# Kernel optimization log

Measured on AMD Instinct MI355X. Metric: run time of the kernel, lower is better.

## Reference

```python
import jax, jax.numpy as jnp
import numpy as np

D_MODEL = 256
D_STATE = 16
D_CONV = 4
EXPAND = 2
D_INNER = EXPAND * D_MODEL  # 512
DT_RANK = (D_MODEL + 15) // 16  # 16
D_FF = 4 * D_MODEL  # 1024
BATCH, SEQ = 16, 2048
EPS = 1e-12


def layer_norm(x, g, b):
    mu = jnp.mean(x, axis=-1, keepdims=True)
    var = jnp.mean(jnp.square(x - mu), axis=-1, keepdims=True)
    return (x - mu) * jax.lax.rsqrt(var + EPS) * g + b


def setup_inputs() -> dict:
    key = jax.random.key(0)
    ks = jax.random.split(key, 16)
    s = lambda n: 1.0 / np.sqrt(n)
    inp = {
        "x": jax.random.normal(ks[0], (BATCH, SEQ, D_MODEL), dtype=jnp.float32),
        "in_proj_w": jax.random.normal(ks[1], (2 * D_INNER, D_MODEL)) * s(D_MODEL),
        "conv_w": jax.random.normal(ks[2], (D_INNER, 1, D_CONV)) * s(D_CONV),
        "conv_b": jax.random.normal(ks[3], (D_INNER,)) * 0.02,
        "x_proj_w": jax.random.normal(ks[4], (DT_RANK + 2 * D_STATE, D_INNER)) * s(D_INNER),
        "dt_proj_w": jax.random.normal(ks[5], (D_INNER, DT_RANK)) * s(DT_RANK),
        "dt_proj_b": jnp.log(jnp.expm1(0.01 * jnp.ones((D_INNER,)))),  # softplus^-1(0.01)
        "A_log": jnp.log(jnp.broadcast_to(jnp.arange(1, D_STATE + 1, dtype=jnp.float32), (D_INNER, D_STATE))),
        "Dskip": jnp.ones((D_INNER,)),
        "out_proj_w": jax.random.normal(ks[6], (D_MODEL, D_INNER)) * s(D_INNER),
        "ln1_g": jnp.ones((D_MODEL,)), "ln1_b": jnp.zeros((D_MODEL,)),
        "w1": jax.random.normal(ks[7], (D_FF, D_MODEL)) * s(D_MODEL),
        "b1": jnp.zeros((D_FF,)),
        "w2": jax.random.normal(ks[8], (D_MODEL, D_FF)) * s(D_FF),
        "b2": jnp.zeros((D_MODEL,)),
        "ln2_g": jnp.ones((D_MODEL,)), "ln2_b": jnp.zeros((D_MODEL,)),
    }
    return inp


def _mamba(x, in_proj_w, conv_w, conv_b, x_proj_w, dt_proj_w, dt_proj_b, A_log, Dskip, out_proj_w):
    B, L, _ = x.shape
    xz = jnp.einsum('bld,ed->ble', x, in_proj_w)  # [B,L,2*D_INNER]
    u, z = jnp.split(xz, 2, axis=-1)
    # depthwise causal conv1d over sequence
    uc = jax.lax.conv_general_dilated(
        u.transpose(0, 2, 1), conv_w, window_strides=(1,),
        padding=[(D_CONV - 1, 0)], feature_group_count=D_INNER,
        dimension_numbers=('NCH', 'OIH', 'NCH'))
    uc = jax.nn.silu(uc + conv_b[None, :, None]).transpose(0, 2, 1)  # [B,L,D_INNER]
    x_dbl = jnp.einsum('blc,ec->ble', uc, x_proj_w)
    dt, Bmat, Cmat = jnp.split(x_dbl, [DT_RANK, DT_RANK + D_STATE], axis=-1)
    delta = jax.nn.softplus(jnp.einsum('blr,cr->blc', dt, dt_proj_w) + dt_proj_b)  # [B,L,D_INNER]
    A = -jnp.exp(A_log)  # [D_INNER, D_STATE]

    def step(h, inp):
        d_t, B_t, C_t, u_t = inp  # [B,dI],[B,N],[B,N],[B,dI]
        dA = jnp.exp(d_t[..., None] * A)                      # [B,dI,N]
        h = h * dA + (d_t * u_t)[..., None] * B_t[:, None, :]  # [B,dI,N]
        y = jnp.sum(h * C_t[:, None, :], axis=-1)              # [B,dI]
        return h, y

    h0 = jnp.zeros((B, D_INNER, D_STATE), dtype=x.dtype)
    xs = (delta.transpose(1, 0, 2), Bmat.transpose(1, 0, 2), Cmat.transpose(1, 0, 2), uc.transpose(1, 0, 2))
    _, ys = jax.lax.scan(step, h0, xs)
    y = ys.transpose(1, 0, 2) + uc * Dskip  # [B,L,D_INNER]
    y = y * jax.nn.silu(z)
    return jnp.einsum('blc,dc->bld', y, out_proj_w)


def reference(x, in_proj_w, conv_w, conv_b, x_proj_w, dt_proj_w, dt_proj_b, A_log, Dskip,
              out_proj_w, ln1_g, ln1_b, w1, b1, w2, b2, ln2_g, ln2_b):
    # MambaLayer.forward, eval mode (dropout = identity), num_layers > 1 -> residual
    h = _mamba(x, in_proj_w, conv_w, conv_b, x_proj_w, dt_proj_w, dt_proj_b, A_log, Dskip, out_proj_w)
    h = layer_norm(h + x, ln1_g, ln1_b)
    # FeedForward: GELU MLP with residual + LayerNorm
    ff = jax.nn.gelu(jnp.einsum('bld,fd->blf', h, w1) + b1, approximate=False)
    ff = jnp.einsum('blf,df->bld', ff, w2) + b2
    return layer_norm(ff + h, ln2_g, ln2_b)
```

## Files before the change

### kernel.cpp

```cpp
#include <hip/hip_runtime.h>
#include <cmath>

#define S_TOTAL 32768
#define LSEQ    2048
#define NBATCH  16
#define DM      256
#define DI      512
#define DSTATE  16
#define DTRANK  16
#define NCHUNK  16
#define CHUNK   128

typedef __attribute__((ext_vector_type(8))) short short8;
typedef __attribute__((ext_vector_type(4))) float f32x4;

__device__ __forceinline__ unsigned short f2bf(float f) {
    union { float f; unsigned int u; } v; v.f = f;
    const unsigned int r = v.u + 0x7fffu + ((v.u >> 16) & 1u);
    return (unsigned short)(r >> 16);
}
__device__ __forceinline__ float bf2f(unsigned short h) {
    union { unsigned int u; float f; } v; v.u = ((unsigned int)h) << 16;
    return v.f;
}
__device__ __forceinline__ float gelu_exact(float x) {
    return 0.5f * x * (1.0f + erff(x * 0.70710678118654752440f));
}
__device__ __forceinline__ float softplus_fast(float x) {
    return fmaxf(x, 0.0f) + __logf(1.0f + __expf(-fabsf(x)));
}

enum { EPI_NONE = 0, EPI_GELU_BIAS = 1, EPI_RESID16 = 2, EPI_BIAS_RESID16 = 3 };

template <int EPI, bool OUTBF>
__global__ __launch_bounds__(256, 4) void gemm_bf16(
    const unsigned short* __restrict__ A, int lda,
    const unsigned short* __restrict__ W, int ldw,
    const float* __restrict__ bias,
    const unsigned short* __restrict__ resid, int ldr,
    void* __restrict__ Cout, int ldc, int nstore,
    int K, int nclampW)
{
    __shared__ unsigned short lds[2][2][4096];

    const int tid = threadIdx.x;
    const int w = tid >> 6, l = tid & 63;
    const int brow = blockIdx.y * 128, bcol = blockIdx.x * 128;
    const int wr = w >> 1, wc = w & 1;
    const int lr = l & 15, lh = l >> 4;

    f32x4 acc[4][4];
    #pragma unroll
    for (int m = 0; m < 4; ++m)
        #pragma unroll
        for (int n = 0; n < 4; ++n)
            acc[m][n] = f32x4{0.f, 0.f, 0.f, 0.f};

    auto stage = [&](int buf, int k0) {
        const int gslot = (l & 3) ^ ((l >> 2) & 3) ^ ((l >> 4) & 3);
        #pragma unroll
        for (int i = 0; i < 2; ++i) {
            const int row = i * 64 + w * 16 + (l >> 2);
            {
                const unsigned short* g =
                    A + (size_t)(brow + row) * lda + k0 + gslot * 8;
                const unsigned short* lp = &lds[buf][0][i * 2048 + w * 512];
                __builtin_amdgcn_global_load_lds(
                    (const __attribute__((address_space(1))) void*)g,
                    (__attribute__((address_space(3))) void*)lp, 16, 0, 0);
            }
            {
                int grow = bcol + row; if (grow > nclampW) grow = nclampW;
                const unsigned short* g =
                    W + (size_t)grow * ldw + k0 + gslot * 8;
                const unsigned short* lp = &lds[buf][1][i * 2048 + w * 512];
                __builtin_amdgcn_global_load_lds(
                    (const __attribute__((address_space(1))) void*)g,
                    (__attribute__((address_space(3))) void*)lp, 16, 0, 0);
            }
        }
    };

    stage(0, 0);

    const int nkt = K >> 5;
    for (int t = 0; t < nkt; ++t) {
        if (t + 1 < nkt) {
            stage((t + 1) & 1, (t + 1) << 5);
            __builtin_amdgcn_sched_barrier(0);
            asm volatile("s_waitcnt vmcnt(4)" ::: "memory");
        } else {
            __builtin_amdgcn_sched_barrier(0);
            asm volatile("s_waitcnt vmcnt(0)" ::: "memory");
        }
        __builtin_amdgcn_s_barrier();
        __builtin_amdgcn_sched_barrier(0);

        const unsigned short* la = &lds[t & 1][0][0];
        const unsigned short* lb = &lds[t & 1][1][0];
        short8 af[4], bw[4];
        #pragma unroll
        for (int m = 0; m < 4; ++m) {
            const int row = wr * 64 + m * 16 + lr;
            const int slot = lh ^ (row & 3) ^ ((row >> 2) & 3);
            af[m] = *(const short8*)(la + row * 32 + slot * 8);
        }
        #pragma unroll
        for (int n = 0; n < 4; ++n) {
            const int row = wc * 64 + n * 16 + lr;
            const int slot = lh ^ (row & 3) ^ ((row >> 2) & 3);
            bw[n] = *(const short8*)(lb + row * 32 + slot * 8);
        }
        #pragma unroll
        for (int m = 0; m < 4; ++m)
            #pragma unroll
            for (int n = 0; n < 4; ++n)
                acc[m][n] = __builtin_amdgcn_mfma_f32_16x16x32_bf16(
                    af[m], bw[n], acc[m][n], 0, 0, 0);

        __builtin_amdgcn_sched_barrier(0);
        asm volatile("s_waitcnt lgkmcnt(0)" ::: "memory");
        __builtin_amdgcn_s_barrier();
        __builtin_amdgcn_sched_barrier(0);
    }

    #pragma unroll
    for (int m = 0; m < 4; ++m) {
        #pragma unroll
        for (int j = 0; j < 4; ++j) {
            const int rg = brow + wr * 64 + m * 16 + lh * 4 + j;
            #pragma unroll
            for (int n = 0; n < 4; ++n) {
                const int cg = bcol + wc * 64 + n * 16 + lr;
                if (cg < nstore) {
                    float v = acc[m][n][j];
                    if (EPI == EPI_GELU_BIAS) {
                        v = gelu_exact(v + bias[cg]);
                    } else if (EPI == EPI_RESID16) {
                        v += bf2f(resid[(size_t)rg * ldr + cg]);
                    } else if (EPI == EPI_BIAS_RESID16) {
                        v += bias[cg] + bf2f(resid[(size_t)rg * ldr + cg]);
                    }
                    if (OUTBF)
                        ((unsigned short*)Cout)[(size_t)rg * ldc + cg] = f2bf(v);
                    else
                        ((float*)Cout)[(size_t)rg * ldc + cg] = v;
                }
            }
        }
    }
}

__global__ __launch_bounds__(256) void convert_kernel(
    const float* __restrict__ x,   const float* __restrict__ win,
    const float* __restrict__ wxp, const float* __restrict__ wop,
    const float* __restrict__ w1,  const float* __restrict__ w2,
    unsigned short* __restrict__ x16, unsigned short* __restrict__ wb)
{
    int idx = blockIdx.x * 256 + threadIdx.x;
    const int NX = S_TOTAL * DM;
    if (idx < NX) { x16[idx] = f2bf(x[idx]); return; }
    idx -= NX;
    if (idx < 262144) { wb[idx] = f2bf(win[idx]); return; }
    idx -= 262144;
    if (idx < 24576)  { wb[262144 + idx] = f2bf(wxp[idx]); return; }
    idx -= 24576;
    if (idx < 131072) { wb[286720 + idx] = f2bf(wop[idx]); return; }
    idx -= 131072;
    if (idx < 262144) { wb[417792 + idx] = f2bf(w1[idx]); return; }
    idx -= 262144;
    if (idx < 262144) { wb[679936 + idx] = f2bf(w2[idx]); return; }
}

__global__ __launch_bounds__(256) void conv_silu_kernel(
    const unsigned short* __restrict__ uz, const float* __restrict__ cw,
    const float* __restrict__ cb, unsigned short* __restrict__ uch)
{
    const int idx = blockIdx.x * 256 + threadIdx.x;
    const int g = idx & 63;
    const int s = idx >> 6;
    const int l = s & (LSEQ - 1);
    const int c0 = g * 8;

    float acc[8];
    float4 cwv[8];
    #pragma unroll
    for (int j = 0; j < 8; ++j) {
        acc[j] = cb[c0 + j];
        cwv[j] = *(const float4*)(cw + (c0 + j) * 4);
    }
    #pragma unroll
    for (int t = 0; t < 4; ++t) {
        const int lt = l - 3 + t;
        if (lt >= 0) {
            const short8 uv = *(const short8*)(uz + (s - 3 + t) * 1024 + c0);
            #pragma unroll
            for (int j = 0; j < 8; ++j) {
                const float wt = (t == 0) ? cwv[j].x : (t == 1) ? cwv[j].y
                               : (t == 2) ? cwv[j].z : cwv[j].w;
                acc[j] += bf2f((unsigned short)uv[j]) * wt;
            }
        }
    }
    short8 ob;
    #pragma unroll
    for (int j = 0; j < 8; ++j) {
        const float sig = 1.0f / (1.0f + __expf(-acc[j]));
        ob[j] = (short)f2bf(acc[j] * sig);
    }
    *(short8*)(uch + s * DI + c0) = ob;
}

__global__ __launch_bounds__(256) void scan_p1(
    const unsigned short* __restrict__ uch, const float* __restrict__ xdbl,
    const float* __restrict__ dtw, const float* __restrict__ dtb,
    const float* __restrict__ A_log,
    float* __restrict__ P, float* __restrict__ Q)
{
    const int tid = threadIdx.x;
    const int cg = blockIdx.x & 7, k = (blockIdx.x >> 3) & 15, b = blockIdx.x >> 7;
    const int c = (cg << 6) + (tid >> 2), nq = (tid & 3) << 2;

    const float4 al = *(const float4*)(A_log + c * DSTATE + nq);
    const float4 a4 = {-__expf(al.x), -__expf(al.y), -__expf(al.z), -__expf(al.w)};
    const float4 dw4 = *(const float4*)(dtw + c * DTRANK + nq);
    const float dtbc = dtb[c];

    float4 h4 = {0, 0, 0, 0};
    float sumd = 0.f;

    const int base = (b * LSEQ + k * CHUNK) * DI + c;
    const int xb   = (b * LSEQ + k * CHUNK) * 64 + nq;

    float  uA_ = bf2f(uch[base]);
    float4 TA_ = *(const float4*)(xdbl + xb);
    float4 BA_ = *(const float4*)(xdbl + xb + DTRANK);
    float  uB_ = bf2f(uch[base + DI]);
    float4 TB_ = *(const float4*)(xdbl + xb + 64);
    float4 BB_ = *(const float4*)(xdbl + xb + 64 + DTRANK);

    for (int l = 0; l < CHUNK; l += 2) {
        const int lc = (l + 2 < CHUNK) ? (l + 2) : (CHUNK - 2);
        const int o2 = base + lc * DI;
        const int x2 = xb + lc * 64;
        const float  uC_ = bf2f(uch[o2]);
        const float  uD_ = bf2f(uch[o2 + DI]);
        const float4 TC_ = *(const float4*)(xdbl + x2);
        const float4 BC_ = *(const float4*)(xdbl + x2 + DTRANK);
        const float4 TD_ = *(const float4*)(xdbl + x2 + 64);
        const float4 BD_ = *(const float4*)(xdbl + x2 + 64 + DTRANK);

        {
            float pd = TA_.x * dw4.x + TA_.y * dw4.y + TA_.z * dw4.z + TA_.w * dw4.w;
            pd += __shfl_xor(pd, 1);
            pd += __shfl_xor(pd, 2);
            const float d = softplus_fast(pd + dtbc);
            const float4 e = {__expf(d * a4.x), __expf(d * a4.y),
                              __expf(d * a4.z), __expf(d * a4.w)};
            const float du = d * uA_;
            h4.x = h4.x * e.x + du * BA_.x;
            h4.y = h4.y * e.y + du * BA_.y;
            h4.z = h4.z * e.z + du * BA_.z;
            h4.w = h4.w * e.w + du * BA_.w;
            sumd += d;
        }
        {
            float pd = TB_.x * dw4.x + TB_.y * dw4.y + TB_.z * dw4.z + TB_.w * dw4.w;
            pd += __shfl_xor(pd, 1);
            pd += __shfl_xor(pd, 2);
            const float d = softplus_fast(pd + dtbc);
            const float4 e = {__expf(d * a4.x), __expf(d * a4.y),
                              __expf(d * a4.z), __expf(d * a4.w)};
            const float du = d * uB_;
            h4.x = h4.x * e.x + du * BB_.x;
            h4.y = h4.y * e.y + du * BB_.y;
            h4.z = h4.z * e.z + du * BB_.z;
            h4.w = h4.w * e.w + du * BB_.w;
            sumd += d;
        }
        uA_ = uC_; TA_ = TC_; BA_ = BC_;
        uB_ = uD_; TB_ = TD_; BB_ = BD_;
    }

    const int pi = ((b * NCHUNK + k) * DI + c) * 16 + nq;
    const float4 P4 = {__expf(a4.x * sumd), __expf(a4.y * sumd),
                       __expf(a4.z * sumd), __expf(a4.w * sumd)};
    *(float4*)(P + pi) = P4;
    *(float4*)(Q + pi) = h4;
}

__global__ __launch_bounds__(256) void scan_p2(
    const float* __restrict__ P, const float* __restrict__ Q,
    float* __restrict__ HS)
{
    const int t  = blockIdx.x * 256 + threadIdx.x;
    const int nq = (t & 3) << 2;
    const int c  = (t >> 2) & (DI - 1);
    const int b  = t >> 11;
    float4 hs = {0, 0, 0, 0};
    for (int k = 0; k < NCHUNK; ++k) {
        const int idx = ((b * NCHUNK + k) * DI + c) * 16 + nq;
        if (k > 0) {
            const int ip = idx - DI * 16;
            const float4 p4 = *(const float4*)(P + ip);
            const float4 q4 = *(const float4*)(Q + ip);
            hs.x = hs.x * p4.x + q4.x;
            hs.y = hs.y * p4.y + q4.y;
            hs.z = hs.z * p4.z + q4.z;
            hs.w = hs.w * p4.w + q4.w;
        }
        *(float4*)(HS + idx) = hs;
    }
}

__global__ __launch_bounds__(256) void scan_p3(
    const unsigned short* __restrict__ uch, const float* __restrict__ xdbl,
    const float* __restrict__ dtw, const float* __restrict__ dtb,
    const unsigned short* __restrict__ zuz,
    const float* __restrict__ A_log, const float* __restrict__ Dskip,
    const float* __restrict__ HS, unsigned short* __restrict__ y)
{
    const int tid = threadIdx.x;
    const int cg = blockIdx.x & 7, k = (blockIdx.x >> 3) & 15, b = blockIdx.x >> 7;
    const int c = (cg << 6) + (tid >> 2), nq = (tid & 3) << 2;

    const float4 al = *(const float4*)(A_log + c * DSTATE + nq);
    const float4 a4 = {-__expf(al.x), -__expf(al.y), -__expf(al.z), -__expf(al.w)};
    const float4 dw4 = *(const float4*)(dtw + c * DTRANK + nq);
    const float dtbc = dtb[c];
    const float dsk = Dskip[c];

    const int pi = ((b * NCHUNK + k) * DI + c) * 16 + nq;
    float4 h4 = *(const float4*)(HS + pi);

    const int base = (b * LSEQ + k * CHUNK) * DI + c;
    const int xb   = (b * LSEQ + k * CHUNK) * 64 + nq;
    const int zb   = (b * LSEQ + k * CHUNK) * 1024 + c;

    float  uA_ = bf2f(uch[base]);
    float  zA_ = bf2f(zuz[zb]);
    float4 TA_ = *(const float4*)(xdbl + xb);
    float4 BA_ = *(const float4*)(xdbl + xb + DTRANK);
    float4 CA_ = *(const float4*)(xdbl + xb + 32);
    float  uB_ = bf2f(uch[base + DI]);
    float  zB_ = bf2f(zuz[zb + 1024]);
    float4 TB_ = *(const float4*)(xdbl + xb + 64);
    float4 BB_ = *(const float4*)(xdbl + xb + 64 + DTRANK);
    float4 CB_ = *(const float4*)(xdbl + xb + 64 + 32);

    for (int l = 0; l < CHUNK; l += 2) {
        const int lc = (l + 2 < CHUNK) ? (l + 2) : (CHUNK - 2);
        const int o2 = base + lc * DI;
        const int x2 = xb + lc * 64;
        const int z2 = zb + lc * 1024;
        const float  uC_ = bf2f(uch[o2]);
        const float  uD_ = bf2f(uch[o2 + DI]);
        const float  zC_ = bf2f(zuz[z2]);
        const float  zD_ = bf2f(zuz[z2 + 1024]);
        const float4 TC_ = *(const float4*)(xdbl + x2);
        const float4 BC_ = *(const float4*)(xdbl + x2 + DTRANK);
        const float4 CC_ = *(const float4*)(xdbl + x2 + 32);
        const float4 TD_ = *(const float4*)(xdbl + x2 + 64);
        const float4 BD_ = *(const float4*)(xdbl + x2 + 64 + DTRANK);
        const float4 CD_ = *(const float4*)(xdbl + x2 + 64 + 32);

        {
            float pd = TA_.x * dw4.x + TA_.y * dw4.y + TA_.z * dw4.z + TA_.w * dw4.w;
            pd += __shfl_xor(pd, 1);
            pd += __shfl_xor(pd, 2);
            const float d = softplus_fast(pd + dtbc);
            const float4 e = {__expf(d * a4.x), __expf(d * a4.y),
                              __expf(d * a4.z), __expf(d * a4.w)};
            const float du = d * uA_;
            h4.x = h4.x * e.x + du * BA_.x;
            h4.y = h4.y * e.y + du * BA_.y;
            h4.z = h4.z * e.z + du * BA_.z;
            h4.w = h4.w * e.w + du * BA_.w;
            float yp = h4.x * CA_.x + h4.y * CA_.y + h4.z * CA_.z + h4.w * CA_.w;
            yp += __shfl_xor(yp, 1);
            yp += __shfl_xor(yp, 2);
            if ((tid & 3) == 0) {
                const float sg = 1.0f / (1.0f + __expf(-zA_));
                y[base + l * DI] = f2bf((yp + uA_ * dsk) * (zA_ * sg));
            }
        }
        {
            float pd = TB_.x * dw4.x + TB_.y * dw4.y + TB_.z * dw4.z + TB_.w * dw4.w;
            pd += __shfl_xor(pd, 1);
            pd += __shfl_xor(pd, 2);
            const float d = softplus_fast(pd + dtbc);
            const float4 e = {__expf(d * a4.x), __expf(d * a4.y),
                              __expf(d * a4.z), __expf(d * a4.w)};
            const float du = d * uB_;
            h4.x = h4.x * e.x + du * BB_.x;
            h4.y = h4.y * e.y + du * BB_.y;
            h4.z = h4.z * e.z + du * BB_.z;
            h4.w = h4.w * e.w + du * BB_.w;
            float yp = h4.x * CB_.x + h4.y * CB_.y + h4.z * CB_.z + h4.w * CB_.w;
            yp += __shfl_xor(yp, 1);
            yp += __shfl_xor(yp, 2);
            if ((tid & 3) == 0) {
                const float sg = 1.0f / (1.0f + __expf(-zB_));
                y[base + (l + 1) * DI] = f2bf((yp + uB_ * dsk) * (zB_ * sg));
            }
        }
        uA_ = uC_; zA_ = zC_; TA_ = TC_; BA_ = BC_; CA_ = CC_;
        uB_ = uD_; zB_ = zD_; TB_ = TD_; BB_ = BD_; CB_ = CD_;
    }
}

__global__ __launch_bounds__(256) void layernorm256_kernel(
    const float* __restrict__ in, const float* __restrict__ g,
    const float* __restrict__ b, float* __restrict__ out,
    unsigned short* __restrict__ out16)
{
    const int wave = threadIdx.x >> 6;
    const int lane = threadIdx.x & 63;
    const int row  = blockIdx.x * 4 + wave;

    const float4 v = ((const float4*)(in + (size_t)row * DM))[lane];
    float s  = v.x + v.y + v.z + v.w;
    float sq = v.x * v.x + v.y * v.y + v.z * v.z + v.w * v.w;
    #pragma unroll
    for (int o = 1; o < 64; o <<= 1) {
        s  += __shfl_xor(s, o);
        sq += __shfl_xor(sq, o);
    }
    const float mu  = s * (1.0f / 256.0f);
    const float var = sq * (1.0f / 256.0f) - mu * mu;
    const float rs  = rsqrtf(var + 1e-12f);

    const float4 gg = ((const float4*)g)[lane];
    const float4 bb = ((const float4*)b)[lane];
    float4 o4;
    o4.x = (v.x - mu) * rs * gg.x + bb.x;
    o4.y = (v.y - mu) * rs * gg.y + bb.y;
    o4.z = (v.z - mu) * rs * gg.z + bb.z;
    o4.w = (v.w - mu) * rs * gg.w + bb.w;
    if (out)
        ((float4*)(out + (size_t)row * DM))[lane] = o4;
    if (out16) {
        uint2 p;
        p.x = (unsigned int)f2bf(o4.x) | ((unsigned int)f2bf(o4.y) << 16);
        p.y = (unsigned int)f2bf(o4.z) | ((unsigned int)f2bf(o4.w) << 16);
        *(uint2*)(out16 + (size_t)row * DM + lane * 4) = p;
    }
}

extern "C" void kernel_launch(void* const* d_in, const int* in_sizes, int n_in,
                              void* d_out, int out_size, void* d_ws, size_t ws_size,
                              hipStream_t stream)
{
    const float* x          = (const float*)d_in[0];
    const float* in_proj_w  = (const float*)d_in[1];
    const float* conv_w     = (const float*)d_in[2];
    const float* conv_b     = (const float*)d_in[3];
    const float* x_proj_w   = (const float*)d_in[4];
    const float* dt_proj_w  = (const float*)d_in[5];
    const float* dt_proj_b  = (const float*)d_in[6];
    const float* A_log      = (const float*)d_in[7];
    const float* Dskip      = (const float*)d_in[8];
    const float* out_proj_w = (const float*)d_in[9];
    const float* ln1_g      = (const float*)d_in[10];
    const float* ln1_b      = (const float*)d_in[11];
    const float* w1         = (const float*)d_in[12];
    const float* b1         = (const float*)d_in[13];
    const float* w2         = (const float*)d_in[14];
    const float* b2         = (const float*)d_in[15];
    const float* ln2_g      = (const float*)d_in[16];
    const float* ln2_b      = (const float*)d_in[17];
    float* out = (float*)d_out;
    char*  ws8 = (char*)d_ws;

    const size_t Mi = 1048576;
    unsigned short* bufUZ  = (unsigned short*)(ws8);
    unsigned short* bufUCh = (unsigned short*)(ws8 + 64 * Mi);
    float*          bufXD  = (float*)(ws8 + 96 * Mi);
    unsigned short* bufFF  = (unsigned short*)(ws8 + 104 * Mi);
    float*          bufP   = (float*)(ws8 + 168 * Mi);
    float*          bufQ   = (float*)(ws8 + 176 * Mi);
    float*          bufHS  = (float*)(ws8 + 184 * Mi);
    unsigned short* wb     = (unsigned short*)(ws8 + 192 * Mi);

    float*          bufM   = (float*)(ws8);
    float*          bufF2  = (float*)(ws8 + 32 * Mi);
    unsigned short* bufH1h = (unsigned short*)(ws8 + 168 * Mi);
    unsigned short* bufY   = bufUCh;

    unsigned short* wInP16 = wb;
    unsigned short* wXP16  = wb + 262144;
    unsigned short* wOP16  = wb + 286720;
    unsigned short* wW116  = wb + 417792;
    unsigned short* wW216  = wb + 679936;

    unsigned short* x16 = (unsigned short*)d_out;

    const dim3 blk(256);
    const int MT = S_TOTAL / 128;

    convert_kernel<<<dim3(36448), blk, 0, stream>>>(
        x, in_proj_w, x_proj_w, out_proj_w, w1, w2, x16, wb);

    gemm_bf16<EPI_NONE, true><<<dim3(8, MT), blk, 0, stream>>>(
        x16, DM, wInP16, DM, nullptr, nullptr, 0, bufUZ, 1024, 1024, DM, 1023);

    conv_silu_kernel<<<dim3(S_TOTAL * 64 / 256), blk, 0, stream>>>(
        bufUZ, conv_w, conv_b, bufUCh);

    gemm_bf16<EPI_NONE, false><<<dim3(1, MT), blk, 0, stream>>>(
        bufUCh, DI, wXP16, DI, nullptr, nullptr, 0, bufXD, 64, 64, DI, 47);

    scan_p1<<<dim3(NBATCH * NCHUNK * 8), blk, 0, stream>>>(
        bufUCh, bufXD, dt_proj_w, dt_proj_b, A_log, bufP, bufQ);
    scan_p2<<<dim3(NBATCH * DI * 4 / 256), blk, 0, stream>>>(
        bufP, bufQ, bufHS);
    scan_p3<<<dim3(NBATCH * NCHUNK * 8), blk, 0, stream>>>(
        bufUCh, bufXD, dt_proj_w, dt_proj_b, bufUZ + 512, A_log, Dskip,
        bufHS, bufY);

    gemm_bf16<EPI_RESID16, false><<<dim3(2, MT), blk, 0, stream>>>(
        bufY, DI, wOP16, DI, nullptr, x16, DM, bufM, DM, 256, DI, 255);

    layernorm256_kernel<<<dim3(S_TOTAL / 4), blk, 0, stream>>>(
        bufM, ln1_g, ln1_b, nullptr, bufH1h);

    gemm_bf16<EPI_GELU_BIAS, true><<<dim3(8, MT), blk, 0, stream>>>(
        bufH1h, DM, wW116, DM, b1, nullptr, 0, bufFF, 1024, 1024, DM, 1023);

    gemm_bf16<EPI_BIAS_RESID16, false><<<dim3(2, MT), blk, 0, stream>>>(
        bufFF, 1024, wW216, 1024, b2, bufH1h, DM, bufF2, DM, 256, 1024, 255);

    layernorm256_kernel<<<dim3(S_TOTAL / 4), blk, 0, stream>>>(
        bufF2, ln2_g, ln2_b, out, nullptr);
}
```

Measured before the change: 647.7 us.

## Precompute delta via a softplus GEMM and restructure scan for more chunks

Delta is now computed once by a new bf16 GEMM (dt_proj with fused softplus-bias epilogue) on the low-rank part of x_proj output, which the x_proj GEMM also writes as bf16 through a new aux output. The scan kernels read precomputed bf16 delta instead of recomputing the dt dot product, softplus and shuffles in both passes. The scan now uses 64-step chunks (32 chunks) with 2 lanes per channel, each holding 8 states, which reduces per-step shuffles and doubles the chunk parallelism. In exchange it adds an extra kernel and bf16 rounding of delta, and it writes and reads a 32MB delta buffer.

```diff
diff --git a/kernel.cpp b/kernel.cpp
--- a/kernel.cpp
+++ b/kernel.cpp
@@ -8,8 +8,8 @@
 #define DI      512
 #define DSTATE  16
 #define DTRANK  16
-#define NCHUNK  16
-#define CHUNK   128
+#define NCHUNK  32
+#define CHUNK   64
 
 typedef __attribute__((ext_vector_type(8))) short short8;
 typedef __attribute__((ext_vector_type(4))) float f32x4;
@@ -30,7 +30,8 @@
     return fmaxf(x, 0.0f) + __logf(1.0f + __expf(-fabsf(x)));
 }
 
-enum { EPI_NONE = 0, EPI_GELU_BIAS = 1, EPI_RESID16 = 2, EPI_BIAS_RESID16 = 3 };
+enum { EPI_NONE = 0, EPI_GELU_BIAS = 1, EPI_RESID16 = 2, EPI_BIAS_RESID16 = 3,
+       EPI_SOFTPLUS_BIAS = 4 };
 
 template <int EPI, bool OUTBF>
 __global__ __launch_bounds__(256, 4) void gemm_bf16(
@@ -39,7 +40,8 @@
     const float* __restrict__ bias,
     const unsigned short* __restrict__ resid, int ldr,
     void* __restrict__ Cout, int ldc, int nstore,
-    int K, int nclampW)
+    int K, int nclampW,
+    unsigned short* __restrict__ aux, int auxn)
 {
     __shared__ unsigned short lds[2][2][4096];
 
@@ -140,11 +142,15 @@
                         v += bf2f(resid[(size_t)rg * ldr + cg]);
                     } else if (EPI == EPI_BIAS_RESID16) {
                         v += bias[cg] + bf2f(resid[(size_t)rg * ldr + cg]);
+                    } else if (EPI == EPI_SOFTPLUS_BIAS) {
+                        v = softplus_fast(v + bias[cg]);
                     }
                     if (OUTBF)
                         ((unsigned short*)Cout)[(size_t)rg * ldc + cg] = f2bf(v);
                     else
                         ((float*)Cout)[(size_t)rg * ldc + cg] = v;
+                    if (aux && cg < auxn)
+                        aux[(size_t)rg * auxn + cg] = f2bf(v);
                 }
             }
         }
@@ -155,6 +161,7 @@
     const float* __restrict__ x,   const float* __restrict__ win,
     const float* __restrict__ wxp, const float* __restrict__ wop,
     const float* __restrict__ w1,  const float* __restrict__ w2,
+    const float* __restrict__ dtw,
     unsigned short* __restrict__ x16, unsigned short* __restrict__ wb)
 {
     int idx = blockIdx.x * 256 + threadIdx.x;
@@ -170,6 +177,12 @@
     if (idx < 262144) { wb[417792 + idx] = f2bf(w1[idx]); return; }
     idx -= 262144;
     if (idx < 262144) { wb[679936 + idx] = f2bf(w2[idx]); return; }
+    idx -= 262144;
+    if (idx < 16384) {
+        const int r = idx >> 5, q = idx & 31;
+        wb[942080 + idx] = (q < DTRANK) ? f2bf(dtw[r * DTRANK + q])
+                                        : (unsigned short)0;
+    }
 }
 
 __global__ __launch_bounds__(256) void conv_silu_kernel(
@@ -212,81 +225,75 @@
 }
 
 __global__ __launch_bounds__(256) void scan_p1(
-    const unsigned short* __restrict__ uch, const float* __restrict__ xdbl,
-    const float* __restrict__ dtw, const float* __restrict__ dtb,
-    const float* __restrict__ A_log,
+    const unsigned short* __restrict__ uch,
+    const unsigned short* __restrict__ delh,
+    const float* __restrict__ xdbl, const float* __restrict__ A_log,
     float* __restrict__ P, float* __restrict__ Q)
 {
     const int tid = threadIdx.x;
-    const int cg = blockIdx.x & 7, k = (blockIdx.x >> 3) & 15, b = blockIdx.x >> 7;
-    const int c = (cg << 6) + (tid >> 2), nq = (tid & 3) << 2;
-
-    const float4 al = *(const float4*)(A_log + c * DSTATE + nq);
-    const float4 a4 = {-__expf(al.x), -__expf(al.y), -__expf(al.z), -__expf(al.w)};
-    const float4 dw4 = *(const float4*)(dtw + c * DTRANK + nq);
-    const float dtbc = dtb[c];
-
-    float4 h4 = {0, 0, 0, 0};
+    const int w = tid >> 6, lane = tid & 63;
+    const int cgb = blockIdx.x & 3;
+    const int k = (blockIdx.x >> 2) & (NCHUNK - 1);
+    const int b = blockIdx.x >> 7;
+    const int c = cgb * 128 + w * 32 + (lane >> 1);
+    const int nb = (lane & 1) * 8;
+
+    float a4[8];
+    {
+        const float4 a0 = *(const float4*)(A_log + c * DSTATE + nb);
+        const float4 a1 = *(const float4*)(A_log + c * DSTATE + nb + 4);
+        a4[0] = -__expf(a0.x); a4[1] = -__expf(a0.y);
+        a4[2] = -__expf(a0.z); a4[3] = -__expf(a0.w);
+        a4[4] = -__expf(a1.x); a4[5] = -__expf(a1.y);
+        a4[6] = -__expf(a1.z); a4[7] = -__expf(a1.w);
+    }
+    float h[8] = {};
     float sumd = 0.f;
 
-    const int base = (b * LSEQ + k * CHUNK) * DI + c;
-    const int xb   = (b * LSEQ + k * CHUNK) * 64 + nq;
-
-    float  uA_ = bf2f(uch[base]);
-    float4 TA_ = *(const float4*)(xdbl + xb);
-    float4 BA_ = *(const float4*)(xdbl + xb + DTRANK);
-    float  uB_ = bf2f(uch[base + DI]);
-    float4 TB_ = *(const float4*)(xdbl + xb + 64);
-    float4 BB_ = *(const float4*)(xdbl + xb + 64 + DTRANK);
+    const int s0 = b * LSEQ + k * CHUNK;
+    const unsigned short* pu = uch + s0 * DI + c;
+    const unsigned short* pd = delh + s0 * DI + c;
+    const float* px = xdbl + s0 * 64 + DTRANK + nb;
+
+    unsigned short dA = pd[0], uA = pu[0];
+    float BA[8];
+    *(float4*)&BA[0] = *(const float4*)(px);
+    *(float4*)&BA[4] = *(const float4*)(px + 4);
 
     for (int l = 0; l < CHUNK; l += 2) {
-        const int lc = (l + 2 < CHUNK) ? (l + 2) : (CHUNK - 2);
-        const int o2 = base + lc * DI;
-        const int x2 = xb + lc * 64;
-        const float  uC_ = bf2f(uch[o2]);
-        const float  uD_ = bf2f(uch[o2 + DI]);
-        const float4 TC_ = *(const float4*)(xdbl + x2);
-        const float4 BC_ = *(const float4*)(xdbl + x2 + DTRANK);
-        const float4 TD_ = *(const float4*)(xdbl + x2 + 64);
-        const float4 BD_ = *(const float4*)(xdbl + x2 + 64 + DTRANK);
-
+        const unsigned short dB = pd[DI], uB = pu[DI];
+        float BB[8];
+        *(float4*)&BB[0] = *(const float4*)(px + 64);
+        *(float4*)&BB[4] = *(const float4*)(px + 68);
         {
-            float pd = TA_.x * dw4.x + TA_.y * dw4.y + TA_.z * dw4.z + TA_.w * dw4.w;
-            pd += __shfl_xor(pd, 1);
-            pd += __shfl_xor(pd, 2);
-            const float d = softplus_fast(pd + dtbc);
-            const float4 e = {__expf(d * a4.x), __expf(d * a4.y),
-                              __expf(d * a4.z), __expf(d * a4.w)};
-            const float du = d * uA_;
-            h4.x = h4.x * e.x + du * BA_.x;
-            h4.y = h4.y * e.y + du * BA_.y;
-            h4.z = h4.z * e.z + du * BA_.z;
-            h4.w = h4.w * e.w + du * BA_.w;
+            const float d = bf2f(dA), u = bf2f(uA);
+            const float du = d * u;
+            #pragma unroll
+            for (int i = 0; i < 8; ++i)
+                h[i] = h[i] * __expf(d * a4[i]) + du * BA[i];
             sumd += d;
         }
+        pu += 2 * DI; pd += 2 * DI; px += 128;
+        dA = pd[0]; uA = pu[0];
+        *(float4*)&BA[0] = *(const float4*)(px);
+        *(float4*)&BA[4] = *(const float4*)(px + 4);
         {
-            float pd = TB_.x * dw4.x + TB_.y * dw4.y + TB_.z * dw4.z + TB_.w * dw4.w;
-            pd += __shfl_xor(pd, 1);
-            pd += __shfl_xor(pd, 2);
-            const float d = softplus_fast(pd + dtbc);
-            const float4 e = {__expf(d * a4.x), __expf(d * a4.y),
-                              __expf(d * a4.z), __expf(d * a4.w)};
-            const float du = d * uB_;
-            h4.x = h4.x * e.x + du * BB_.x;
-            h4.y = h4.y * e.y + du * BB_.y;
-            h4.z = h4.z * e.z + du * BB_.z;
-            h4.w = h4.w * e.w + du * BB_.w;
+            const float d = bf2f(dB), u = bf2f(uB);
+            const float du = d * u;
+            #pragma unroll
+            for (int i = 0; i < 8; ++i)
+                h[i] = h[i] * __expf(d * a4[i]) + du * BB[i];
             sumd += d;
         }
-        uA_ = uC_; TA_ = TC_; BA_ = BC_;
-        uB_ = uD_; TB_ = TD_; BB_ = BD_;
-    }
-
-    const int pi = ((b * NCHUNK + k) * DI + c) * 16 + nq;
-    const float4 P4 = {__expf(a4.x * sumd), __expf(a4.y * sumd),
-                       __expf(a4.z * sumd), __expf(a4.w * sumd)};
-    *(float4*)(P + pi) = P4;
-    *(float4*)(Q + pi) = h4;
+    }
+
+    const int pi = ((b * NCHUNK + k) * DI + c) * 16 + nb;
+    *(float4*)(P + pi) = make_float4(__expf(a4[0] * sumd), __expf(a4[1] * sumd),
+                                     __expf(a4[2] * sumd), __expf(a4[3] * sumd));
+    *(float4*)(P + pi + 4) = make_float4(__expf(a4[4] * sumd), __expf(a4[5] * sumd),
+                                         __expf(a4[6] * sumd), __expf(a4[7] * sumd));
+    *(float4*)(Q + pi) = make_float4(h[0], h[1], h[2], h[3]);
+    *(float4*)(Q + pi + 4) = make_float4(h[4], h[5], h[6], h[7]);
 }
 
 __global__ __launch_bounds__(256) void scan_p2(
@@ -314,98 +321,94 @@
 }
 
 __global__ __launch_bounds__(256) void scan_p3(
-    const unsigned short* __restrict__ uch, const float* __restrict__ xdbl,
-    const float* __restrict__ dtw, const float* __restrict__ dtb,
-    const unsigned short* __restrict__ zuz,
+    const unsigned short* __restrict__ uch,
+    const unsigned short* __restrict__ delh,
+    const float* __restrict__ xdbl, const unsigned short* __restrict__ zuz,
     const float* __restrict__ A_log, const float* __restrict__ Dskip,
     const float* __restrict__ HS, unsigned short* __restrict__ y)
 {
     const int tid = threadIdx.x;
-    const int cg = blockIdx.x & 7, k = (blockIdx.x >> 3) & 15, b = blockIdx.x >> 7;
-    const int c = (cg << 6) + (tid >> 2), nq = (tid & 3) << 2;
-
-    const float4 al = *(const float4*)(A_log + c * DSTATE + nq);
-    const float4 a4 = {-__expf(al.x), -__expf(al.y), -__expf(al.z), -__expf(al.w)};
-    const float4 dw4 = *(const float4*)(dtw + c * DTRANK + nq);
-    const float dtbc = dtb[c];
+    const int w = tid >> 6, lane = tid & 63;
+    const int cgb = blockIdx.x & 3;
+    const int k = (blockIdx.x >> 2) & (NCHUNK - 1);
+    const int b = blockIdx.x >> 7;
+    const int c = cgb * 128 + w * 32 + (lane >> 1);
+    const int nb = (lane & 1) * 8;
+
+    float a4[8];
+    {
+        const float4 a0 = *(const float4*)(A_log + c * DSTATE + nb);
+        const float4 a1 = *(const float4*)(A_log + c * DSTATE + nb + 4);
+        a4[0] = -__expf(a0.x); a4[1] = -__expf(a0.y);
+        a4[2] = -__expf(a0.z); a4[3] = -__expf(a0.w);
+        a4[4] = -__expf(a1.x); a4[5] = -__expf(a1.y);
+        a4[6] = -__expf(a1.z); a4[7] = -__expf(a1.w);
+    }
     const float dsk = Dskip[c];
 
-    const int pi = ((b * NCHUNK + k) * DI + c) * 16 + nq;
-    float4 h4 = *(const float4*)(HS + pi);
-
-    const int base = (b * LSEQ + k * CHUNK) * DI + c;
-    const int xb   = (b * LSEQ + k * CHUNK) * 64 + nq;
-    const int zb   = (b * LSEQ + k * CHUNK) * 1024 + c;
-
-    float  uA_ = bf2f(uch[base]);
-    float  zA_ = bf2f(zuz[zb]);
-    float4 TA_ = *(const float4*)(xdbl + xb);
-    float4 BA_ = *(const float4*)(xdbl + xb + DTRANK);
-    float4 CA_ = *(const float4*)(xdbl + xb + 32);
-    float  uB_ = bf2f(uch[base + DI]);
-    float  zB_ = bf2f(zuz[zb + 1024]);
-    float4 TB_ = *(const float4*)(xdbl + xb + 64);
-    float4 BB_ = *(const float4*)(xdbl + xb + 64 + DTRANK);
-    float4 CB_ = *(const float4*)(xdbl + xb + 64 + 32);
+    const int pi = ((b * NCHUNK + k) * DI + c) * 16 + nb;
+    float h[8];
+    *(float4*)&h[0] = *(const float4*)(HS + pi);
+    *(float4*)&h[4] = *(const float4*)(HS + pi + 4);
+
+    const int s0 = b * LSEQ + k * CHUNK;
+    const unsigned short* pu = uch + s0 * DI + c;
+    const unsigned short* pd = delh + s0 * DI + c;
+    const unsigned short* pz = zuz + s0 * 1024 + c;
+    const float* px = xdbl + s0 * 64 + DTRANK + nb;
+    unsigned short* py = y + s0 * DI + c;
+
+    unsigned short dA = pd[0], uA = pu[0], zA = pz[0];
+    float BA[8], CA[8];
+    *(float4*)&BA[0] = *(const float4*)(px);
+    *(float4*)&BA[4] = *(const float4*)(px + 4);
+    *(float4*)&CA[0] = *(const float4*)(px + DSTATE);
+    *(float4*)&CA[4] = *(const float4*)(px + DSTATE + 4);
 
     for (int l = 0; l < CHUNK; l += 2) {
-        const int lc = (l + 2 < CHUNK) ? (l + 2) : (CHUNK - 2);
-        const int o2 = base + lc * DI;
-        const int x2 = xb + lc * 64;
-        const int z2 = zb + lc * 1024;
-        const float  uC_ = bf2f(uch[o2]);
-        const float  uD_ = bf2f(uch[o2 + DI]);
-        const float  zC_ = bf2f(zuz[z2]);
-        const float  zD_ = bf2f(zuz[z2 + 1024]);
-        const float4 TC_ = *(const float4*)(xdbl + x2);
-        const float4 BC_ = *(const float4*)(xdbl + x2 + DTRANK);
-        const float4 CC_ = *(const float4*)(xdbl + x2 + 32);
-        const float4 TD_ = *(const float4*)(xdbl + x2 + 64);
-        const float4 BD_ = *(const float4*)(xdbl + x2 + 64 + DTRANK);
-        const float4 CD_ = *(const float4*)(xdbl + x2 + 64 + 32);
-
+        const unsigned short dB = pd[DI], uB = pu[DI], zB = pz[1024];
+        float BB[8], CB[8];
+        *(float4*)&BB[0] = *(const float4*)(px + 64);
+        *(float4*)&BB[4] = *(const float4*)(px + 68);
+        *(float4*)&CB[0] = *(const float4*)(px + 64 + DSTATE);
+        *(float4*)&CB[4] = *(const float4*)(px + 68 + DSTATE);
         {
-            float pd = TA_.x * dw4.x + TA_.y * dw4.y + TA_.z * dw4.z + TA_.w * dw4.w;
-            pd += __shfl_xor(pd, 1);
-            pd += __shfl_xor(pd, 2);
-            const float d = softplus_fast(pd + dtbc);
-            const float4 e = {__expf(d * a4.x), __expf(d * a4.y),
-                              __expf(d * a4.z), __expf(d * a4.w)};
-            const float du = d * uA_;
-            h4.x = h4.x * e.x + du * BA_.x;
-            h4.y = h4.y * e.y + du * BA_.y;
-            h4.z = h4.z * e.z + du * BA_.z;
-            h4.w = h4.w * e.w + du * BA_.w;
-            float yp = h4.x * CA_.x + h4.y * CA_.y + h4.z * CA_.z + h4.w * CA_.w;
+            const float d = bf2f(dA), u = bf2f(uA), z = bf2f(zA);
+            const float du = d * u;
+            float yp = 0.f;
+            #pragma unroll
+            for (int i = 0; i < 8; ++i) {
+                h[i] = h[i] * __expf(d * a4[i]) + du * BA[i];
+                yp += h[i] * CA[i];
+            }
             yp += __shfl_xor(yp, 1);
-            yp += __shfl_xor(yp, 2);
-            if ((tid & 3) == 0) {
-                const float sg = 1.0f / (1.0f + __expf(-zA_));
-                y[base + l * DI] = f2bf((yp + uA_ * dsk) * (zA_ * sg));
-            }
-        }
+            if ((lane & 1) == 0) {
+                const float sg = __builtin_amdgcn_rcpf(1.0f + __expf(-z));
+                py[0] = f2bf((yp + u * dsk) * (z * sg));
+            }
+        }
+        pu += 2 * DI; pd += 2 * DI; pz += 2048; px += 128;
+        dA = pd[0]; uA = pu[0]; zA = pz[0];
+        *(float4*)&BA[0] = *(const float4*)(px);
+        *(float4*)&BA[4] = *(const float4*)(px + 4);
+        *(float4*)&CA[0] = *(const float4*)(px + DSTATE);
+        *(float4*)&CA[4] = *(const float4*)(px + DSTATE + 4);
         {
-            float pd = TB_.x * dw4.x + TB_.y * dw4.y + TB_.z * dw4.z + TB_.w * dw4.w;
-            pd += __shfl_xor(pd, 1);
-            pd += __shfl_xor(pd, 2);
-            const float d = softplus_fast(pd + dtbc);
-            const float4 e = {__expf(d * a4.x), __expf(d * a4.y),
-                              __expf(d * a4.z), __expf(d * a4.w)};
-            const float du = d * uB_;
-            h4.x = h4.x * e.x + du * BB_.x;
-            h4.y = h4.y * e.y + du * BB_.y;
-            h4.z = h4.z * e.z + du * BB_.z;
-            h4.w = h4.w * e.w + du * BB_.w;
-            float yp = h4.x * CB_.x + h4.y * CB_.y + h4.z * CB_.z + h4.w * CB_.w;
+            const float d = bf2f(dB), u = bf2f(uB), z = bf2f(zB);
+            const float du = d * u;
+            float yp = 0.f;
+            #pragma unroll
+            for (int i = 0; i < 8; ++i) {
+                h[i] = h[i] * __expf(d * a4[i]) + du * BB[i];
+                yp += h[i] * CB[i];
+            }
             yp += __shfl_xor(yp, 1);
-            yp += __shfl_xor(yp, 2);
-            if ((tid & 3) == 0) {
-                const float sg = 1.0f / (1.0f + __expf(-zB_));
-                y[base + (l + 1) * DI] = f2bf((yp + uB_ * dsk) * (zB_ * sg));
-            }
-        }
-        uA_ = uC_; zA_ = zC_; TA_ = TC_; BA_ = BC_; CA_ = CC_;
-        uB_ = uD_; zB_ = zD_; TB_ = TD_; BB_ = BD_; CB_ = CD_;
+            if ((lane & 1) == 0) {
+                const float sg = __builtin_amdgcn_rcpf(1.0f + __expf(-z));
+                py[DI] = f2bf((yp + u * dsk) * (z * sg));
+            }
+        }
+        py += 2 * DI;
     }
 }
 
@@ -477,14 +480,16 @@
     unsigned short* bufUCh = (unsigned short*)(ws8 + 64 * Mi);
     float*          bufXD  = (float*)(ws8 + 96 * Mi);
     unsigned short* bufFF  = (unsigned short*)(ws8 + 104 * Mi);
-    float*          bufP   = (float*)(ws8 + 168 * Mi);
-    float*          bufQ   = (float*)(ws8 + 176 * Mi);
-    float*          bufHS  = (float*)(ws8 + 184 * Mi);
-    unsigned short* wb     = (unsigned short*)(ws8 + 192 * Mi);
+    float*          bufP   = (float*)(ws8 + 104 * Mi);
+    float*          bufQ   = (float*)(ws8 + 120 * Mi);
+    float*          bufHS  = (float*)(ws8 + 136 * Mi);
+    unsigned short* bufH1h = (unsigned short*)(ws8 + 168 * Mi);
+    unsigned short* bufXDh = (unsigned short*)(ws8 + 184 * Mi);
+    unsigned short* bufDelh= (unsigned short*)(ws8 + 186 * Mi);
+    unsigned short* wb     = (unsigned short*)(ws8 + 218 * Mi);
 
     float*          bufM   = (float*)(ws8);
     float*          bufF2  = (float*)(ws8 + 32 * Mi);
-    unsigned short* bufH1h = (unsigned short*)(ws8 + 168 * Mi);
     unsigned short* bufY   = bufUCh;
 
     unsigned short* wInP16 = wb;
@@ -492,43 +497,52 @@
     unsigned short* wOP16  = wb + 286720;
     unsigned short* wW116  = wb + 417792;
     unsigned short* wW216  = wb + 679936;
+    unsigned short* wDTp16 = wb + 942080;
 
     unsigned short* x16 = (unsigned short*)d_out;
 
     const dim3 blk(256);
     const int MT = S_TOTAL / 128;
 
-    convert_kernel<<<dim3(36448), blk, 0, stream>>>(
-        x, in_proj_w, x_proj_w, out_proj_w, w1, w2, x16, wb);
+    convert_kernel<<<dim3(36512), blk, 0, stream>>>(
+        x, in_proj_w, x_proj_w, out_proj_w, w1, w2, dt_proj_w, x16, wb);
 
     gemm_bf16<EPI_NONE, true><<<dim3(8, MT), blk, 0, stream>>>(
-        x16, DM, wInP16, DM, nullptr, nullptr, 0, bufUZ, 1024, 1024, DM, 1023);
+        x16, DM, wInP16, DM, nullptr, nullptr, 0, bufUZ, 1024, 1024, DM, 1023,
+        nullptr, 0);
 
     conv_silu_kernel<<<dim3(S_TOTAL * 64 / 256), blk, 0, stream>>>(
         bufUZ, conv_w, conv_b, bufUCh);
 
     gemm_bf16<EPI_NONE, false><<<dim3(1, MT), blk, 0, stream>>>(
-        bufUCh, DI, wXP16, DI, nullptr, nullptr, 0, bufXD, 64, 64, DI, 47);
-
-    scan_p1<<<dim3(NBATCH * NCHUNK * 8), blk, 0, stream>>>(
-        bufUCh, bufXD, dt_proj_w, dt_proj_b, A_log, bufP, bufQ);
-    scan_p2<<<dim3(NBATCH * DI * 4 / 256), blk, 0, stream>>>(
+        bufUCh, DI, wXP16, DI, nullptr, nullptr, 0, bufXD, 64, 48, DI, 47,
+        bufXDh, 32);
+
+    gemm_bf16<EPI_SOFTPLUS_BIAS, true><<<dim3(4, MT), blk, 0, stream>>>(
+        bufXDh, 32, wDTp16, 32, dt_proj_b, nullptr, 0, bufDelh, DI, DI, 32, 511,
+        nullptr, 0);
+
+    scan_p1<<<dim3(NBATCH * NCHUNK * 4), blk, 0, stream>>>(
+        bufUCh, bufDelh, bufXD, A_log, bufP, bufQ);
+    scan_p2<<<dim3(S_TOTAL / 256), blk, 0, stream>>>(
         bufP, bufQ, bufHS);
-    scan_p3<<<dim3(NBATCH * NCHUNK * 8), blk, 0, stream>>>(
-        bufUCh, bufXD, dt_proj_w, dt_proj_b, bufUZ + 512, A_log, Dskip,
-        bufHS, bufY);
+    scan_p3<<<dim3(NBATCH * NCHUNK * 4), blk, 0, stream>>>(
+        bufUCh, bufDelh, bufXD, bufUZ + 512, A_log, Dskip, bufHS, bufY);
 
     gemm_bf16<EPI_RESID16, false><<<dim3(2, MT), blk, 0, stream>>>(
-        bufY, DI, wOP16, DI, nullptr, x16, DM, bufM, DM, 256, DI, 255);
+        bufY, DI, wOP16, DI, nullptr, x16, DM, bufM, DM, 256, DI, 255,
+        nullptr, 0);
 
     layernorm256_kernel<<<dim3(S_TOTAL / 4), blk, 0, stream>>>(
         bufM, ln1_g, ln1_b, nullptr, bufH1h);
 
     gemm_bf16<EPI_GELU_BIAS, true><<<dim3(8, MT), blk, 0, stream>>>(
-        bufH1h, DM, wW116, DM, b1, nullptr, 0, bufFF, 1024, 1024, DM, 1023);
+        bufH1h, DM, wW116, DM, b1, nullptr, 0, bufFF, 1024, 1024, DM, 1023,
+        nullptr, 0);
 
     gemm_bf16<EPI_BIAS_RESID16, false><<<dim3(2, MT), blk, 0, stream>>>(
-        bufFF, 1024, wW216, 1024, b2, bufH1h, DM, bufF2, DM, 256, 1024, 255);
+        bufFF, 1024, wW216, 1024, b2, bufH1h, DM, bufF2, DM, 256, 1024, 255,
+        nullptr, 0);
 
     layernorm256_kernel<<<dim3(S_TOTAL / 4), blk, 0, stream>>>(
         bufF2, ln2_g, ln2_b, out, nullptr);
```

After: 566.2 us. 12.6% less time.
